# Kernel optimization log

Measured on AMD Instinct MI355X. Metric: run time of the kernel, lower is better.

The kernel has to match this reference:

```python
import jax, jax.numpy as jnp
import numpy as np

EPS = 1e-9

def setup_inputs() -> dict:
    key = jax.random.key(0)
    k1, k2 = jax.random.split(key)
    h = jax.random.normal(k1, (16384, 4096), dtype=jnp.float32)
    W = jax.random.normal(k2, (64, 4096), dtype=jnp.float32) * 0.02  # nn.Linear weight [n_experts, d]
    return {"h": h, "W": W}

def reference(h, W):
    k = 2
    # logits: [tokens, n_experts]
    logits = jnp.einsum('td,ed->te', h, W)
    weights_full = jax.nn.softmax(logits, axis=-1)
    # top-k on logits (torch.topk returns sorted descending, as does lax.top_k)
    _, idx = jax.lax.top_k(logits, k)  # idx: [tokens, k]
    # masked renormalization: since top-k indices are distinct, the masked sum
    # equals the sum of gathered softmax weights
    gathered = jnp.take_along_axis(weights_full, idx, axis=-1)  # [tokens, k]
    weights_topk = gathered / (jnp.sum(gathered, axis=-1, keepdims=True) + EPS)
    return weights_topk, idx
```

## Files before the change

kernel.cpp:

```cpp
#include <hip/hip_runtime.h>
#include <math.h>

#define DIM   4096
#define NEXP  64
#define MB    32
#define KC    128
#define NST   (DIM / KC)

typedef _Float16 f16x8 __attribute__((ext_vector_type(8)));
typedef _Float16 f16x4 __attribute__((ext_vector_type(4)));
typedef float    f32x4 __attribute__((ext_vector_type(4)));

__global__ __launch_bounds__(256)
void pack_w_kernel(const float* __restrict__ W,
                   _Float16* __restrict__ wph, _Float16* __restrict__ wpl) {
    const int flat = blockIdx.x * 256 + threadIdx.x;
    const int lane = flat & 63;
    const int ck   = (flat >> 6) & 127;
    const int nt   = flat >> 13;
    const int e    = nt * 16 + (lane & 15);
    const int k0   = ck * 32 + (lane >> 4) * 8;
    const float* src = W + ((size_t)e << 12) + k0;
    float4 v0 = *(const float4*)(src);
    float4 v1 = *(const float4*)(src + 4);
    float vv[8] = {v0.x, v0.y, v0.z, v0.w, v1.x, v1.y, v1.z, v1.w};
    f16x8 hi, lo;
#pragma unroll
    for (int i = 0; i < 8; ++i) {
        _Float16 hh = (_Float16)vv[i];
        hi[i] = hh;
        lo[i] = (_Float16)(vv[i] - (float)hh);
    }
    *(f16x8*)(wph + (size_t)flat * 8) = hi;
    *(f16x8*)(wpl + (size_t)flat * 8) = lo;
}

__global__ __launch_bounds__(256, 3)
void gate_mfma_kernel(const float* __restrict__ h,
                      const _Float16* __restrict__ wph,
                      const _Float16* __restrict__ wpl,
                      float* __restrict__ out, int n_tokens) {
    __shared__ _Float16 Ah[2][MB * KC];
    __shared__ _Float16 Al[2][MB * KC];
    __shared__ float    lg[MB][NEXP + 4];

    const int tid  = threadIdx.x;
    const int lane = tid & 63;
    const int wv   = __builtin_amdgcn_readfirstlane(tid >> 6);
    const int l15  = lane & 15;
    const int quad = lane >> 4;
    const int t0   = blockIdx.x * MB;

    int s_t[4], s_q[4];
    float4 st[4];
#pragma unroll
    for (int r = 0; r < 4; ++r) {
        int flat = r * 256 + tid;
        s_t[r] = flat >> 5;
        s_q[r] = flat & 31;
        st[r]  = *(const float4*)(h + (size_t)(t0 + s_t[r]) * DIM + 4 * s_q[r]);
    }

    const _Float16* bph = wph + ((size_t)(wv * 128) * 64 + lane) * 8;
    const _Float16* bpl = wpl + ((size_t)(wv * 128) * 64 + lane) * 8;
    f16x8 Bh[2][4], Bl[2][4];
#pragma unroll
    for (int s = 0; s < 4; ++s) {
        Bh[0][s] = *(const f16x8*)(bph + s * 512);
        Bl[0][s] = *(const f16x8*)(bpl + s * 512);
    }

    f32x4 acc0 = {0.f, 0.f, 0.f, 0.f};
    f32x4 acc1 = {0.f, 0.f, 0.f, 0.f};

#pragma unroll 2
    for (int c = 0; c < NST; ++c) {
        const int buf = c & 1;
#pragma unroll
        for (int r = 0; r < 4; ++r) {
            float4 v = st[r];
            _Float16 a0 = (_Float16)v.x, a1 = (_Float16)v.y,
                     a2 = (_Float16)v.z, a3 = (_Float16)v.w;
            f16x4 hh = {a0, a1, a2, a3};
            f16x4 ll = {(_Float16)(v.x - (float)a0), (_Float16)(v.y - (float)a1),
                        (_Float16)(v.z - (float)a2), (_Float16)(v.w - (float)a3)};
            int t = s_t[r], q = s_q[r];
            int addr = t * KC + (((q >> 1) ^ (t & 15)) << 3) + ((q & 1) << 2);
            *(f16x4*)(&Ah[buf][addr]) = hh;
            *(f16x4*)(&Al[buf][addr]) = ll;
        }
        __syncthreads();

        if (c + 1 < NST) {
            const int kn = (c + 1) * KC;
#pragma unroll
            for (int r = 0; r < 4; ++r)
                st[r] = *(const float4*)(h + (size_t)(t0 + s_t[r]) * DIM + kn + 4 * s_q[r]);
            const int nb = (c + 1) & 1;
            const size_t coff = (size_t)(c + 1) * 4 * 512;
#pragma unroll
            for (int s = 0; s < 4; ++s) {
                Bh[nb][s] = *(const f16x8*)(bph + coff + s * 512);
                Bl[nb][s] = *(const f16x8*)(bpl + coff + s * 512);
            }
        }

#pragma unroll
        for (int s = 0; s < 4; ++s) {
            const int pb = (((4 * s + quad) ^ l15) << 3);
            f16x8 a0h = *(const f16x8*)(&Ah[buf][l15 * KC + pb]);
            f16x8 a1h = *(const f16x8*)(&Ah[buf][(16 + l15) * KC + pb]);
            f16x8 a0l = *(const f16x8*)(&Al[buf][l15 * KC + pb]);
            f16x8 a1l = *(const f16x8*)(&Al[buf][(16 + l15) * KC + pb]);
            f16x8 bh = Bh[buf][s], bl = Bl[buf][s];
            acc0 = __builtin_amdgcn_mfma_f32_16x16x32_f16(a0h, bh, acc0, 0, 0, 0);
            acc1 = __builtin_amdgcn_mfma_f32_16x16x32_f16(a1h, bh, acc1, 0, 0, 0);
            acc0 = __builtin_amdgcn_mfma_f32_16x16x32_f16(a0l, bh, acc0, 0, 0, 0);
            acc1 = __builtin_amdgcn_mfma_f32_16x16x32_f16(a1l, bh, acc1, 0, 0, 0);
            acc0 = __builtin_amdgcn_mfma_f32_16x16x32_f16(a0h, bl, acc0, 0, 0, 0);
            acc1 = __builtin_amdgcn_mfma_f32_16x16x32_f16(a1h, bl, acc1, 0, 0, 0);
        }
    }

#pragma unroll
    for (int r = 0; r < 4; ++r) {
        lg[4 * quad + r][wv * 16 + l15]      = acc0[r];
        lg[16 + 4 * quad + r][wv * 16 + l15] = acc1[r];
    }
    __syncthreads();

    if (tid < MB) {
        const float* row = lg[tid];
        float m = -INFINITY;
#pragma unroll 8
        for (int e = 0; e < NEXP; ++e) m = fmaxf(m, row[e]);
        float z = 0.0f, b1 = -INFINITY, b2 = -INFINITY;
        int i1 = 0, i2 = 0;
        for (int e = 0; e < NEXP; ++e) {
            float v = row[e];
            z += expf(v - m);
            if (v > b1)      { b2 = b1; i2 = i1; b1 = v; i1 = e; }
            else if (v > b2) { b2 = v; i2 = e; }
        }
        float g1 = expf(b1 - m), g2 = expf(b2 - m);
        float w1 = g1 / z, w2 = g2 / z;
        float ssum = w1 + w2 + 1e-9f;
        int t = t0 + tid;
        *(float2*)(out + 2 * t) = make_float2(w1 / ssum, w2 / ssum);
        *(float2*)(out + 2 * n_tokens + 2 * t) = make_float2((float)i1, (float)i2);
    }
}

extern "C" void kernel_launch(void* const* d_in, const int* in_sizes, int n_in,
                              void* d_out, int out_size, void* d_ws, size_t ws_size,
                              hipStream_t stream) {
    const float* h = (const float*)d_in[0];
    const float* W = (const float*)d_in[1];
    float* out = (float*)d_out;
    const int n_tokens = in_sizes[0] / DIM;

    _Float16* wph = (_Float16*)d_ws;
    _Float16* wpl = wph + (size_t)NEXP * DIM;

    pack_w_kernel<<<(NEXP * DIM / 8) / 256, 256, 0, stream>>>(W, wph, wpl);
    gate_mfma_kernel<<<n_tokens / MB, 256, 0, stream>>>(h, wph, wpl, out, n_tokens);
}
```

Measured before the change: 371.6 us.

## Halve token tile to 16 and prefetch h two chunks ahead

Reduces the token tile per block from 32 to 16, so each wave computes one 16x16 MFMA tile instead of two, and raises the occupancy hint from 3 to 4 blocks per CU. The h loads are now prefetched two K-chunks ahead into a double-buffered register array, deepening the global-load pipeline. This doubles the block count and exposes more memory parallelism for the bandwidth-bound h stream. In exchange, each block's W fragments in registers are reused across half as many tokens, so W traffic from L2 doubles.

```diff
diff --git a/kernel.cpp b/kernel.cpp
--- a/kernel.cpp
+++ b/kernel.cpp
@@ -3,7 +3,7 @@
 
 #define DIM   4096
 #define NEXP  64
-#define MB    32
+#define MB    16
 #define KC    128
 #define NST   (DIM / KC)
 
@@ -35,7 +35,7 @@
     *(f16x8*)(wpl + (size_t)flat * 8) = lo;
 }
 
-__global__ __launch_bounds__(256, 3)
+__global__ __launch_bounds__(256, 4)
 void gate_mfma_kernel(const float* __restrict__ h,
                       const _Float16* __restrict__ wph,
                       const _Float16* __restrict__ wpl,
@@ -51,15 +51,21 @@
     const int quad = lane >> 4;
     const int t0   = blockIdx.x * MB;
 
-    int s_t[4], s_q[4];
-    float4 st[4];
+    int s_t[2], s_f4[2];
 #pragma unroll
-    for (int r = 0; r < 4; ++r) {
-        int flat = r * 256 + tid;
-        s_t[r] = flat >> 5;
-        s_q[r] = flat & 31;
-        st[r]  = *(const float4*)(h + (size_t)(t0 + s_t[r]) * DIM + 4 * s_q[r]);
+    for (int d = 0; d < 2; ++d) {
+        int flat = d * 256 + tid;
+        s_t[d]  = flat >> 5;
+        s_f4[d] = flat & 31;
     }
+    const float* hrow0 = h + (size_t)(t0 + s_t[0]) * DIM + 4 * s_f4[0];
+    const float* hrow1 = h + (size_t)(t0 + s_t[1]) * DIM + 4 * s_f4[1];
+
+    float4 st[2][2];
+    st[0][0] = *(const float4*)(hrow0);
+    st[0][1] = *(const float4*)(hrow1);
+    st[1][0] = *(const float4*)(hrow0 + KC);
+    st[1][1] = *(const float4*)(hrow1 + KC);
 
     const _Float16* bph = wph + ((size_t)(wv * 128) * 64 + lane) * 8;
     const _Float16* bpl = wpl + ((size_t)(wv * 128) * 64 + lane) * 8;
@@ -70,32 +76,32 @@
         Bl[0][s] = *(const f16x8*)(bpl + s * 512);
     }
 
-    f32x4 acc0 = {0.f, 0.f, 0.f, 0.f};
-    f32x4 acc1 = {0.f, 0.f, 0.f, 0.f};
+    f32x4 acc = {0.f, 0.f, 0.f, 0.f};
 
 #pragma unroll 2
     for (int c = 0; c < NST; ++c) {
         const int buf = c & 1;
 #pragma unroll
-        for (int r = 0; r < 4; ++r) {
-            float4 v = st[r];
+        for (int d = 0; d < 2; ++d) {
+            float4 v = st[buf][d];
             _Float16 a0 = (_Float16)v.x, a1 = (_Float16)v.y,
                      a2 = (_Float16)v.z, a3 = (_Float16)v.w;
             f16x4 hh = {a0, a1, a2, a3};
             f16x4 ll = {(_Float16)(v.x - (float)a0), (_Float16)(v.y - (float)a1),
                         (_Float16)(v.z - (float)a2), (_Float16)(v.w - (float)a3)};
-            int t = s_t[r], q = s_q[r];
-            int addr = t * KC + (((q >> 1) ^ (t & 15)) << 3) + ((q & 1) << 2);
+            int t = s_t[d], f4 = s_f4[d], b = f4 >> 1;
+            int addr = t * KC + (((b ^ t) & 15) << 3) + ((f4 & 1) << 2);
             *(f16x4*)(&Ah[buf][addr]) = hh;
             *(f16x4*)(&Al[buf][addr]) = ll;
         }
         __syncthreads();
 
+        if (c + 2 < NST) {
+            const int kn = (c + 2) * KC;
+            st[buf][0] = *(const float4*)(hrow0 + kn);
+            st[buf][1] = *(const float4*)(hrow1 + kn);
+        }
         if (c + 1 < NST) {
-            const int kn = (c + 1) * KC;
-#pragma unroll
-            for (int r = 0; r < 4; ++r)
-                st[r] = *(const float4*)(h + (size_t)(t0 + s_t[r]) * DIM + kn + 4 * s_q[r]);
             const int nb = (c + 1) & 1;
             const size_t coff = (size_t)(c + 1) * 4 * 512;
 #pragma unroll
@@ -107,26 +113,19 @@
 
 #pragma unroll
         for (int s = 0; s < 4; ++s) {
-            const int pb = (((4 * s + quad) ^ l15) << 3);
-            f16x8 a0h = *(const f16x8*)(&Ah[buf][l15 * KC + pb]);
-            f16x8 a1h = *(const f16x8*)(&Ah[buf][(16 + l15) * KC + pb]);
-            f16x8 a0l = *(const f16x8*)(&Al[buf][l15 * KC + pb]);
-            f16x8 a1l = *(const f16x8*)(&Al[buf][(16 + l15) * KC + pb]);
+            const int bsw = (((4 * s + quad) ^ l15) & 15) << 3;
+            f16x8 ah = *(const f16x8*)(&Ah[buf][l15 * KC + bsw]);
+            f16x8 al = *(const f16x8*)(&Al[buf][l15 * KC + bsw]);
             f16x8 bh = Bh[buf][s], bl = Bl[buf][s];
-            acc0 = __builtin_amdgcn_mfma_f32_16x16x32_f16(a0h, bh, acc0, 0, 0, 0);
-            acc1 = __builtin_amdgcn_mfma_f32_16x16x32_f16(a1h, bh, acc1, 0, 0, 0);
-            acc0 = __builtin_amdgcn_mfma_f32_16x16x32_f16(a0l, bh, acc0, 0, 0, 0);
-            acc1 = __builtin_amdgcn_mfma_f32_16x16x32_f16(a1l, bh, acc1, 0, 0, 0);
-            acc0 = __builtin_amdgcn_mfma_f32_16x16x32_f16(a0h, bl, acc0, 0, 0, 0);
-            acc1 = __builtin_amdgcn_mfma_f32_16x16x32_f16(a1h, bl, acc1, 0, 0, 0);
+            acc = __builtin_amdgcn_mfma_f32_16x16x32_f16(ah, bh, acc, 0, 0, 0);
+            acc = __builtin_amdgcn_mfma_f32_16x16x32_f16(al, bh, acc, 0, 0, 0);
+            acc = __builtin_amdgcn_mfma_f32_16x16x32_f16(ah, bl, acc, 0, 0, 0);
         }
     }
 
 #pragma unroll
-    for (int r = 0; r < 4; ++r) {
-        lg[4 * quad + r][wv * 16 + l15]      = acc0[r];
-        lg[16 + 4 * quad + r][wv * 16 + l15] = acc1[r];
-    }
+    for (int r = 0; r < 4; ++r)
+        lg[4 * quad + r][wv * 16 + l15] = acc[r];
     __syncthreads();
 
     if (tid < MB) {
```

Result: no change. 377.5 us (+1.6%).
